# Optimization experiments

Hardware: AMD Instinct MI355X
Metric: run time of the kernel (lower is better)

Reference implementation:

```python
import jax, jax.numpy as jnp
import numpy as np

N = 50000      # num nodes
E = 800000     # num edges (avg degree 16)
D = 128        # feature dim
HOP = 2        # number of propagation hops
FILL = 0.5     # self-loop fill value (A_hat = A + fill*I)


def setup_inputs() -> dict:
    key = jax.random.key(0)
    k1, k2, k3, k4, k5 = jax.random.split(key, 5)
    x_s = jax.random.normal(k1, (N, D), dtype=jnp.float32)
    x_t = jax.random.normal(k2, (N, D), dtype=jnp.float32)
    src = jax.random.randint(k3, (E,), 0, N)
    # guarantee no pre-existing self-loops so that appending all self-loops
    # exactly matches add_remaining_self_loops
    dst = (src + jax.random.randint(k4, (E,), 1, N)) % N
    edge_index = jnp.stack([src, dst]).astype(jnp.int32)
    edge_weight = jax.random.uniform(k5, (E,), dtype=jnp.float32)
    # DIMPA parameters, initialized to 1.0 per _reset_parameters
    w_s = jnp.ones((HOP + 1, 1), dtype=jnp.float32)
    w_t = jnp.ones((HOP + 1, 1), dtype=jnp.float32)
    return {"x_s": x_s, "x_t": x_t, "edge_index": edge_index,
            "edge_weight": edge_weight, "w_s": w_s, "w_t": w_t}


def _conv(x, row, col, w, n, fill):
    # Conv_Base: add self loops with weight `fill`, row-normalize by weighted
    # out-degree of `row`, scatter-add messages w_norm * x[row] onto `col`.
    loop = jnp.arange(n, dtype=row.dtype)
    row_a = jnp.concatenate([row, loop])
    col_a = jnp.concatenate([col, loop])
    w_a = jnp.concatenate([w, jnp.full((n,), fill, dtype=w.dtype)])
    deg = jax.ops.segment_sum(w_a, row_a, num_segments=n)
    deg_inv = jnp.where(deg == 0, jnp.zeros_like(deg), 1.0 / deg)  # inf -> 0
    w_norm = deg_inv[row_a] * w_a                                   # [E+n]
    return jax.ops.segment_sum(w_norm[:, None] * x[row_a], col_a, num_segments=n)


def reference(x_s, x_t, edge_index, edge_weight, w_s, w_t):
    n = x_s.shape[0]
    row, col = edge_index[0], edge_index[1]
    feat_s = w_s[0] * x_s
    feat_t = w_t[0] * x_t
    curr_s, curr_t = x_s, x_t
    for h in range(1, HOP + 1):
        curr_s = _conv(curr_s, row, col, edge_weight, n, FILL)
        # edge_index_t = edge_index[[1, 0]] -> swap row/col
        curr_t = _conv(curr_t, col, row, edge_weight, n, FILL)
        feat_s = feat_s + w_s[h] * curr_s
        feat_t = feat_t + w_t[h] * curr_t
    return jnp.concatenate([feat_s, feat_t], axis=1)  # [N, 2D]
```

## Files before the change

kernel.cpp:

```cpp
#include <hip/hip_runtime.h>

#define D 128
#define FILLV 0.5f
#define NXCD 8
#define EPT 8

#define CNT_SHIFT 22
#define DEG_MASK  0x3FFFFFu

typedef unsigned short u16;
typedef unsigned long long u64;
typedef unsigned uv4 __attribute__((ext_vector_type(4)));

__device__ __forceinline__ u16 f2bf(float f) {
    unsigned u = __float_as_uint(f);
    u += 0x7FFF + ((u >> 16) & 1);
    return (u16)(u >> 16);
}
__device__ __forceinline__ float bf2f(u16 h) {
    return __uint_as_float(((unsigned)h) << 16);
}

__global__ void cnt_tobf_kernel(const int* __restrict__ row, const int* __restrict__ col,
                                const float* __restrict__ w,
                                unsigned* __restrict__ cnt32, unsigned* __restrict__ ranks,
                                const float* __restrict__ x_s, const float* __restrict__ x_t,
                                u16* __restrict__ xb_s, u16* __restrict__ xb_t,
                                int E, int N, int nEB, long long nd) {
    if ((int)blockIdx.x < nEB) {
        long long g  = (long long)blockIdx.x * 256 + threadIdx.x;
        long long e0 = g * EPT;
        if (e0 >= E) return;
        if (e0 + EPT <= E && (E & 3) == 0) {
            int rr[EPT]; int cc[EPT]; unsigned fx[EPT];
            #pragma unroll
            for (int h = 0; h < EPT / 4; ++h) {
                int q = (int)(e0 >> 2) + h;
                int4   r4 = *(const int4*)(row + 4 * (size_t)q);
                int4   c4 = *(const int4*)(col + 4 * (size_t)q);
                float4 w4 = *(const float4*)(w + 4 * (size_t)q);
                rr[4*h] = r4.x; rr[4*h+1] = r4.y; rr[4*h+2] = r4.z; rr[4*h+3] = r4.w;
                cc[4*h] = c4.x; cc[4*h+1] = c4.y; cc[4*h+2] = c4.z; cc[4*h+3] = c4.w;
                fx[4*h]   = (unsigned)(w4.x * 65536.0f);
                fx[4*h+1] = (unsigned)(w4.y * 65536.0f);
                fx[4*h+2] = (unsigned)(w4.z * 65536.0f);
                fx[4*h+3] = (unsigned)(w4.w * 65536.0f);
            }
            unsigned oc[EPT], orr[EPT];
            #pragma unroll
            for (int k = 0; k < EPT; ++k) {
                unsigned add = (1u << CNT_SHIFT) | fx[k];
                oc[k]  = atomicAdd(&cnt32[(size_t)cc[k]], add);
                orr[k] = atomicAdd(&cnt32[(size_t)N + rr[k]], add);
            }
            unsigned pk[EPT];
            #pragma unroll
            for (int k = 0; k < EPT; ++k)
                pk[k] = ((orr[k] >> CNT_SHIFT) << 16) | (oc[k] >> CNT_SHIFT);
            uv4 pa = {pk[0], pk[1], pk[2], pk[3]};
            uv4 pb = {pk[4], pk[5], pk[6], pk[7]};
            __builtin_nontemporal_store(pa, (uv4*)(ranks + e0));
            __builtin_nontemporal_store(pb, (uv4*)(ranks + e0 + 4));
        } else {
            for (long long e = e0; e < E && e < e0 + EPT; ++e) {
                int r = row[e], c = col[e];
                unsigned add = (1u << CNT_SHIFT) | (unsigned)(w[e] * 65536.0f);
                unsigned oc  = atomicAdd(&cnt32[(size_t)c], add);
                unsigned orr = atomicAdd(&cnt32[(size_t)N + r], add);
                ranks[e] = ((orr >> CNT_SHIFT) << 16) | (oc >> CNT_SHIFT);
            }
        }
    } else {
        long long t = (long long)(blockIdx.x - nEB) * 256 + threadIdx.x;
        long long q = nd / 4;
        const float* x; u16* xb; long long i;
        if (t < q) { x = x_s; xb = xb_s; i = t * 4; }
        else if (t < 2 * q) { x = x_t; xb = xb_t; i = (t - q) * 4; }
        else return;
        float4 v = *(const float4*)(x + i);
        ushort4 o;
        o.x = f2bf(v.x); o.y = f2bf(v.y); o.z = f2bf(v.z); o.w = f2bf(v.w);
        *(ushort4*)(xb + i) = o;
    }
}

__global__ void scanAI_kernel(unsigned* __restrict__ cnt32, float* __restrict__ dinv,
                              int* __restrict__ tsum, int total) {
    __shared__ int sh[256];
    int gid = blockIdx.x * 256 + threadIdx.x;
    int cnt = 0;
    if (gid < total) {
        unsigned v = cnt32[gid];
        float deg = (float)(v & DEG_MASK) * (1.0f / 65536.0f);
        dinv[gid] = 1.0f / (deg + FILLV);
        cnt = (int)(v >> CNT_SHIFT);
        cnt32[gid] = (unsigned)cnt;
    }
    sh[threadIdx.x] = cnt;
    __syncthreads();
    for (int off = 128; off > 0; off >>= 1) {
        if (threadIdx.x < off) sh[threadIdx.x] += sh[threadIdx.x + off];
        __syncthreads();
    }
    if (threadIdx.x == 0) tsum[blockIdx.x] = sh[0];
}

__global__ void scanC_kernel(const unsigned* __restrict__ cnt32, const int* __restrict__ tsum,
                             int* __restrict__ start, int total, int grand_total) {
    __shared__ int sh[256];
    int acc = 0;
    for (int j = threadIdx.x; j < (int)blockIdx.x; j += 256) acc += tsum[j];
    sh[threadIdx.x] = acc;
    __syncthreads();
    for (int off = 128; off > 0; off >>= 1) {
        if (threadIdx.x < off) sh[threadIdx.x] += sh[threadIdx.x + off];
        __syncthreads();
    }
    int bpref = sh[0];
    __syncthreads();
    int gid = blockIdx.x * 256 + threadIdx.x;
    int v = (gid < total) ? (int)cnt32[gid] : 0;
    sh[threadIdx.x] = v;
    __syncthreads();
    for (int off = 1; off < 256; off <<= 1) {
        int u = 0;
        if (threadIdx.x >= off) u = sh[threadIdx.x - off];
        __syncthreads();
        sh[threadIdx.x] += u;
        __syncthreads();
    }
    int run = bpref + sh[threadIdx.x] - v;
    if (gid < total) start[gid] = run;
    if (gid == 0) start[total] = grand_total;
}

__global__ void slot_kernel(const int* __restrict__ start,
                            const int* __restrict__ row, const int* __restrict__ col,
                            const float* __restrict__ w, const unsigned* __restrict__ ranks,
                            const float* __restrict__ dinv,
                            u64* __restrict__ ssst, u64* __restrict__ es, u64* __restrict__ et,
                            int E, int N) {
    long long g  = (long long)blockIdx.x * blockDim.x + threadIdx.x;
    long long e0 = g * 4;
    if (e0 >= E) return;
    if (e0 + 4 <= E && (E & 3) == 0) {
        int q = (int)(e0 >> 2);
        int4   r4 = *(const int4*)(row + 4 * (size_t)q);
        int4   c4 = *(const int4*)(col + 4 * (size_t)q);
        float4 w4 = *(const float4*)(w + 4 * (size_t)q);
        uv4    p4 = __builtin_nontemporal_load((const uv4*)(ranks + e0));
        int rr[4] = {r4.x, r4.y, r4.z, r4.w};
        int cc[4] = {c4.x, c4.y, c4.z, c4.w};
        float ww[4] = {w4.x, w4.y, w4.z, w4.w};
        unsigned pk[4] = {p4.x, p4.y, p4.z, p4.w};
        #pragma unroll
        for (int k = 0; k < 4; ++k) {
            int ss = start[cc[k]] + (int)(pk[k] & 0xffffu);
            int st = start[N + rr[k]] + (int)(pk[k] >> 16);
            float wns = ww[k] * dinv[N + rr[k]];
            float wnt = ww[k] * dinv[cc[k]];
            u64 sv = ((u64)(unsigned)st << 32) | (unsigned)ss;
            u64 ev = ((u64)__float_as_uint(wns) << 32) | (unsigned)rr[k];
            u64 tv = ((u64)__float_as_uint(wnt) << 32) | (unsigned)cc[k];
            __builtin_nontemporal_store(sv, ssst + e0 + k);
            __builtin_nontemporal_store(ev, es + e0 + k);
            __builtin_nontemporal_store(tv, et + e0 + k);
        }
    } else {
        for (long long e = e0; e < E && e < e0 + 4; ++e) {
            int r = row[e], c = col[e];
            float we = w[e];
            unsigned pk = ranks[e];
            int ss = start[c] + (int)(pk & 0xffffu);
            int st = start[N + r] + (int)(pk >> 16);
            float wns = we * dinv[N + r];
            float wnt = we * dinv[c];
            __builtin_nontemporal_store(((u64)(unsigned)st << 32) | (unsigned)ss, ssst + e);
            __builtin_nontemporal_store(((u64)__float_as_uint(wns) << 32) | (unsigned)r, es + e);
            __builtin_nontemporal_store(((u64)__float_as_uint(wnt) << 32) | (unsigned)c, et + e);
        }
    }
}

__global__ void fillX_kernel(const u64* __restrict__ ssst,
                             const u64* __restrict__ es, const u64* __restrict__ et,
                             u64* __restrict__ edges, int E, int SL) {
    int e = (int)(blockIdx.x >> 3) * blockDim.x + threadIdx.x;
    int rid = blockIdx.x & 7;
    if (e >= E) return;
    int lo = rid * SL, hi = lo + SL;
    u64 sv = __builtin_nontemporal_load(ssst + e);
    int ss = (int)(unsigned)(sv & 0xffffffffu);
    int st = (int)(unsigned)(sv >> 32);
    bool ds = (ss >= lo) & (ss < hi);
    bool dt = (st >= lo) & (st < hi);
    if (ds) {
        u64 ev = __builtin_nontemporal_load(es + e);
        edges[ss] = ev;
    }
    if (dt) {
        u64 tv = __builtin_nontemporal_load(et + e);
        edges[st] = tv;
    }
}

__global__ void pull1_kernel(const int* __restrict__ start, const int2* __restrict__ edges,
                             const float* __restrict__ dinv,
                             const u16* __restrict__ xb_s, const u16* __restrict__ xb_t,
                             const float* __restrict__ x_s, const float* __restrict__ x_t,
                             u16* __restrict__ ab_s, u16* __restrict__ ab_t, int N) {
    int wid0 = (int)(((long long)blockIdx.x * blockDim.x + threadIdx.x) >> 6);
    int wid = __builtin_amdgcn_readfirstlane(wid0);
    int lane = threadIdx.x & 63;
    int half = lane >> 5, hl = lane & 31;
    if (wid >= 2 * N) return;
    const u16* xb; const float* x; u16* ab; int i, o;
    if (wid < N) { i = wid;     o = N; xb = xb_s; x = x_s; ab = ab_s; }
    else         { i = wid - N; o = 0; xb = xb_t; x = x_t; ab = ab_t; }
    int s0 = start[wid], s1 = start[wid + 1];
    float a0 = 0.f, a1 = 0.f, a2 = 0.f, a3 = 0.f;
    int k = s0;
    for (; k + 8 <= s1; k += 8) {
        int b = k + 4 * half;
        int2 p0 = edges[b], p1 = edges[b + 1], p2 = edges[b + 2], p3 = edges[b + 3];
        ushort4 v0 = *(const ushort4*)(xb + (size_t)p0.x * D + hl * 4);
        ushort4 v1 = *(const ushort4*)(xb + (size_t)p1.x * D + hl * 4);
        ushort4 v2 = *(const ushort4*)(xb + (size_t)p2.x * D + hl * 4);
        ushort4 v3 = *(const ushort4*)(xb + (size_t)p3.x * D + hl * 4);
        float w0v = __int_as_float(p0.y), w1v = __int_as_float(p1.y);
        float w2v = __int_as_float(p2.y), w3v = __int_as_float(p3.y);
        a0 += w0v * bf2f(v0.x) + w1v * bf2f(v1.x) + w2v * bf2f(v2.x) + w3v * bf2f(v3.x);
        a1 += w0v * bf2f(v0.y) + w1v * bf2f(v1.y) + w2v * bf2f(v2.y) + w3v * bf2f(v3.y);
        a2 += w0v * bf2f(v0.z) + w1v * bf2f(v1.z) + w2v * bf2f(v2.z) + w3v * bf2f(v3.z);
        a3 += w0v * bf2f(v0.w) + w1v * bf2f(v1.w) + w2v * bf2f(v2.w) + w3v * bf2f(v3.w);
    }
    if (k + 4 <= s1) {
        int b = k + 2 * half;
        int2 p0 = edges[b], p1 = edges[b + 1];
        ushort4 v0 = *(const ushort4*)(xb + (size_t)p0.x * D + hl * 4);
        ushort4 v1 = *(const ushort4*)(xb + (size_t)p1.x * D + hl * 4);
        float w0v = __int_as_float(p0.y), w1v = __int_as_float(p1.y);
        a0 += w0v * bf2f(v0.x) + w1v * bf2f(v1.x);
        a1 += w0v * bf2f(v0.y) + w1v * bf2f(v1.y);
        a2 += w0v * bf2f(v0.z) + w1v * bf2f(v1.z);
        a3 += w0v * bf2f(v0.w) + w1v * bf2f(v1.w);
        k += 4;
    }
    for (; k < s1; ++k) {
        if (half == 0) {
            int2 p = edges[k];
            ushort4 v = *(const ushort4*)(xb + (size_t)p.x * D + hl * 4);
            float wv = __int_as_float(p.y);
            a0 += wv * bf2f(v.x); a1 += wv * bf2f(v.y);
            a2 += wv * bf2f(v.z); a3 += wv * bf2f(v.w);
        }
    }
    a0 += __shfl_xor(a0, 32); a1 += __shfl_xor(a1, 32);
    a2 += __shfl_xor(a2, 32); a3 += __shfl_xor(a3, 32);
    if (half == 0) {
        float sw = FILLV * dinv[o + i];
        float4 xv = *(const float4*)(x + (size_t)i * D + hl * 4);
        a0 += sw * xv.x; a1 += sw * xv.y; a2 += sw * xv.z; a3 += sw * xv.w;
        ushort4 ov;
        ov.x = f2bf(a0); ov.y = f2bf(a1); ov.z = f2bf(a2); ov.w = f2bf(a3);
        *(ushort4*)(ab + (size_t)i * D + hl * 4) = ov;
    }
}

__global__ void pull2_kernel(const int* __restrict__ start, const int2* __restrict__ edges,
                             const float* __restrict__ dinv,
                             const u16* __restrict__ ab_s, const u16* __restrict__ ab_t,
                             const float* __restrict__ x_s, const float* __restrict__ x_t,
                             float* __restrict__ out,
                             const float* __restrict__ w_s, const float* __restrict__ w_t, int N) {
    int wid0 = (int)(((long long)blockIdx.x * blockDim.x + threadIdx.x) >> 6);
    int wid = __builtin_amdgcn_readfirstlane(wid0);
    int lane = threadIdx.x & 63;
    int half = lane >> 5, hl = lane & 31;
    if (wid >= 2 * N) return;
    const u16* ab; const float* x; const float* wv3; int i, o, hoff;
    if (wid < N) { i = wid;     o = N; ab = ab_s; x = x_s; wv3 = w_s; hoff = 0; }
    else         { i = wid - N; o = 0; ab = ab_t; x = x_t; wv3 = w_t; hoff = D; }
    int s0 = start[wid], s1 = start[wid + 1];
    float a0 = 0.f, a1 = 0.f, a2 = 0.f, a3 = 0.f;
    int k = s0;
    for (; k + 8 <= s1; k += 8) {
        int b = k + 4 * half;
        int2 p0 = edges[b], p1 = edges[b + 1], p2 = edges[b + 2], p3 = edges[b + 3];
        ushort4 v0 = *(const ushort4*)(ab + (size_t)p0.x * D + hl * 4);
        ushort4 v1 = *(const ushort4*)(ab + (size_t)p1.x * D + hl * 4);
        ushort4 v2 = *(const ushort4*)(ab + (size_t)p2.x * D + hl * 4);
        ushort4 v3 = *(const ushort4*)(ab + (size_t)p3.x * D + hl * 4);
        float w0v = __int_as_float(p0.y), w1v = __int_as_float(p1.y);
        float w2v = __int_as_float(p2.y), w3v = __int_as_float(p3.y);
        a0 += w0v * bf2f(v0.x) + w1v * bf2f(v1.x) + w2v * bf2f(v2.x) + w3v * bf2f(v3.x);
        a1 += w0v * bf2f(v0.y) + w1v * bf2f(v1.y) + w2v * bf2f(v2.y) + w3v * bf2f(v3.y);
        a2 += w0v * bf2f(v0.z) + w1v * bf2f(v1.z) + w2v * bf2f(v2.z) + w3v * bf2f(v3.z);
        a3 += w0v * bf2f(v0.w) + w1v * bf2f(v1.w) + w2v * bf2f(v2.w) + w3v * bf2f(v3.w);
    }
    if (k + 4 <= s1) {
        int b = k + 2 * half;
        int2 p0 = edges[b], p1 = edges[b + 1];
        ushort4 v0 = *(const ushort4*)(ab + (size_t)p0.x * D + hl * 4);
        ushort4 v1 = *(const ushort4*)(ab + (size_t)p1.x * D + hl * 4);
        float w0v = __int_as_float(p0.y), w1v = __int_as_float(p1.y);
        a0 += w0v * bf2f(v0.x) + w1v * bf2f(v1.x);
        a1 += w0v * bf2f(v0.y) + w1v * bf2f(v1.y);
        a2 += w0v * bf2f(v0.z) + w1v * bf2f(v1.z);
        a3 += w0v * bf2f(v0.w) + w1v * bf2f(v1.w);
        k += 4;
    }
    for (; k < s1; ++k) {
        if (half == 0) {
            int2 p = edges[k];
            ushort4 v = *(const ushort4*)(ab + (size_t)p.x * D + hl * 4);
            float wv = __int_as_float(p.y);
            a0 += wv * bf2f(v.x); a1 += wv * bf2f(v.y);
            a2 += wv * bf2f(v.z); a3 += wv * bf2f(v.w);
        }
    }
    a0 += __shfl_xor(a0, 32); a1 += __shfl_xor(a1, 32);
    a2 += __shfl_xor(a2, 32); a3 += __shfl_xor(a3, 32);
    if (half == 0) {
        float sw = FILLV * dinv[o + i];
        ushort4 av = *(const ushort4*)(ab + (size_t)i * D + hl * 4);
        float b0 = bf2f(av.x), b1 = bf2f(av.y), b2 = bf2f(av.z), b3 = bf2f(av.w);
        a0 += sw * b0; a1 += sw * b1; a2 += sw * b2; a3 += sw * b3;
        float w0 = wv3[0], w1 = wv3[1], w2 = wv3[2];
        float4 xv = *(const float4*)(x + (size_t)i * D + hl * 4);
        float4 ov;
        ov.x = w0 * xv.x + w1 * b0 + w2 * a0;
        ov.y = w0 * xv.y + w1 * b1 + w2 * a1;
        ov.z = w0 * xv.z + w1 * b2 + w2 * a2;
        ov.w = w0 * xv.w + w1 * b3 + w2 * a3;
        *(float4*)(out + (size_t)i * 2 * D + hoff + hl * 4) = ov;
    }
}

extern "C" void kernel_launch(void* const* d_in, const int* in_sizes, int n_in,
                              void* d_out, int out_size, void* d_ws, size_t ws_size,
                              hipStream_t stream) {
    const float* x_s = (const float*)d_in[0];
    const float* x_t = (const float*)d_in[1];
    const int*   ei  = (const int*)d_in[2];
    const float* ew  = (const float*)d_in[3];
    const float* w_s = (const float*)d_in[4];
    const float* w_t = (const float*)d_in[5];
    const int N = in_sizes[0] / D;
    const int E = in_sizes[3];
    const int* row = ei;
    const int* col = ei + E;

    const int total = 2 * N;
    const int nTiles = (total + 255) / 256;

    float* f      = (float*)d_ws;
    float* dinv   = f;
    int*   start  = (int*)(f + (size_t)total);
    int*   tsum   = start + (total + 2);
    char*  pc     = (char*)(tsum + 512);
    pc = (char*)(((size_t)pc + 255) & ~(size_t)255);
    u64*   edges  = (u64*)pc;
    u16*   xb_s   = (u16*)(edges + 2 * (size_t)E);
    u16*   xb_t   = xb_s + (size_t)N * D;
    u16*   ab_s   = xb_t + (size_t)N * D;
    u16*   ab_t   = ab_s + (size_t)N * D;
    unsigned* cnt32 = (unsigned*)ab_s;

    unsigned* ranks = (unsigned*)d_out;
    char* po = (char*)d_out + (((size_t)E * 4 + 15) & ~(size_t)15);
    u64* ssst = (u64*)po;
    u64* es   = ssst + (size_t)E;
    u64* et   = es + (size_t)E;
    float* out = (float*)d_out;

    hipMemsetAsync(cnt32, 0, (size_t)total * sizeof(unsigned), stream);

    long long nd = (long long)N * D;
    int blkC = (int)((nd / 2 + 255) / 256);
    int blkE = (E + 255) / 256;
    int nEB  = (E + EPT * 256 - 1) / (EPT * 256);
    cnt_tobf_kernel<<<nEB + blkC, 256, 0, stream>>>(row, col, ew, cnt32, ranks,
                                                    x_s, x_t, xb_s, xb_t,
                                                    E, N, nEB, nd);
    scanAI_kernel<<<nTiles, 256, 0, stream>>>(cnt32, dinv, tsum, total);
    scanC_kernel<<<nTiles, 256, 0, stream>>>(cnt32, tsum, start, total, 2 * E);

    int blkS = (E / 4 + 256) / 256 + 1;
    slot_kernel<<<blkS, 256, 0, stream>>>(start, row, col, ew, ranks, dinv,
                                          ssst, es, et, E, N);

    int SL = ((2 * E + NXCD - 1) / NXCD + 7) & ~7;
    fillX_kernel<<<NXCD * blkE, 256, 0, stream>>>(ssst, es, et, edges, E, SL);

    long long pull_threads = (long long)total * 64;
    int blkP = (int)((pull_threads + 255) / 256);
    pull1_kernel<<<blkP, 256, 0, stream>>>(start, (const int2*)edges, dinv, xb_s, xb_t,
                                           x_s, x_t, ab_s, ab_t, N);
    pull2_kernel<<<blkP, 256, 0, stream>>>(start, (const int2*)edges, dinv, ab_s, ab_t,
                                           x_s, x_t, out, w_s, w_t, N);
}
```

Measured before the change: 351.8 us.

## Bucket edge records by destination XCD slice before scatter fill

The slot kernel now bins each edge record by which destination range (one per XCD) its CSR slot falls in, using a shared-memory histogram and global atomic cursors, and writes compact per-bin slot and payload arrays. The fill kernel then reads only its own bin instead of having all 8 range-filtered passes re-scan every edge. This removes the 8x redundant reads of the staging arrays but adds atomics and a non-deterministic write order within bins, and it needs extra cursor memset space.

```diff
diff --git a/kernel.cpp b/kernel.cpp
--- a/kernel.cpp
+++ b/kernel.cpp
@@ -11,6 +11,7 @@
 typedef unsigned short u16;
 typedef unsigned long long u64;
 typedef unsigned uv4 __attribute__((ext_vector_type(4)));
+typedef u64 u64v2 __attribute__((ext_vector_type(2)));
 
 __device__ __forceinline__ u16 f2bf(float f) {
     unsigned u = __float_as_uint(f);
@@ -134,73 +135,95 @@
     if (gid == 0) start[total] = grand_total;
 }
 
-__global__ void slot_kernel(const int* __restrict__ start,
-                            const int* __restrict__ row, const int* __restrict__ col,
-                            const float* __restrict__ w, const unsigned* __restrict__ ranks,
-                            const float* __restrict__ dinv,
-                            u64* __restrict__ ssst, u64* __restrict__ es, u64* __restrict__ et,
-                            int E, int N) {
-    long long g  = (long long)blockIdx.x * blockDim.x + threadIdx.x;
+__global__ void slot2_kernel(const int* __restrict__ start,
+                             const int* __restrict__ row, const int* __restrict__ col,
+                             const float* __restrict__ w, const unsigned* __restrict__ ranks,
+                             const float* __restrict__ dinv,
+                             unsigned* __restrict__ cursor,
+                             unsigned* __restrict__ bslot, u64* __restrict__ bpay,
+                             int E, int N, int SL) {
+    __shared__ unsigned hist[NXCD];
+    __shared__ unsigned wbase[NXCD];
+    if (threadIdx.x < NXCD) hist[threadIdx.x] = 0;
+    __syncthreads();
+    long long g  = (long long)blockIdx.x * 256 + threadIdx.x;
     long long e0 = g * 4;
-    if (e0 >= E) return;
-    if (e0 + 4 <= E && (E & 3) == 0) {
-        int q = (int)(e0 >> 2);
-        int4   r4 = *(const int4*)(row + 4 * (size_t)q);
-        int4   c4 = *(const int4*)(col + 4 * (size_t)q);
-        float4 w4 = *(const float4*)(w + 4 * (size_t)q);
-        uv4    p4 = __builtin_nontemporal_load((const uv4*)(ranks + e0));
-        int rr[4] = {r4.x, r4.y, r4.z, r4.w};
-        int cc[4] = {c4.x, c4.y, c4.z, c4.w};
-        float ww[4] = {w4.x, w4.y, w4.z, w4.w};
-        unsigned pk[4] = {p4.x, p4.y, p4.z, p4.w};
-        #pragma unroll
-        for (int k = 0; k < 4; ++k) {
-            int ss = start[cc[k]] + (int)(pk[k] & 0xffffu);
-            int st = start[N + rr[k]] + (int)(pk[k] >> 16);
-            float wns = ww[k] * dinv[N + rr[k]];
-            float wnt = ww[k] * dinv[cc[k]];
-            u64 sv = ((u64)(unsigned)st << 32) | (unsigned)ss;
-            u64 ev = ((u64)__float_as_uint(wns) << 32) | (unsigned)rr[k];
-            u64 tv = ((u64)__float_as_uint(wnt) << 32) | (unsigned)cc[k];
-            __builtin_nontemporal_store(sv, ssst + e0 + k);
-            __builtin_nontemporal_store(ev, es + e0 + k);
-            __builtin_nontemporal_store(tv, et + e0 + k);
+    unsigned rslot[8]; u64 rpay[8]; unsigned rbin[8], rrank[8];
+    int nrec = 0;
+    if (e0 < E) {
+        if (e0 + 4 <= E && (E & 3) == 0) {
+            int q = (int)(e0 >> 2);
+            int4   r4 = *(const int4*)(row + 4 * (size_t)q);
+            int4   c4 = *(const int4*)(col + 4 * (size_t)q);
+            float4 w4 = *(const float4*)(w + 4 * (size_t)q);
+            uv4    p4 = __builtin_nontemporal_load((const uv4*)(ranks + e0));
+            int rr[4] = {r4.x, r4.y, r4.z, r4.w};
+            int cc[4] = {c4.x, c4.y, c4.z, c4.w};
+            float ww[4] = {w4.x, w4.y, w4.z, w4.w};
+            unsigned pk[4] = {p4.x, p4.y, p4.z, p4.w};
+            #pragma unroll
+            for (int k = 0; k < 4; ++k) {
+                int ss = start[cc[k]] + (int)(pk[k] & 0xffffu);
+                int st = start[N + rr[k]] + (int)(pk[k] >> 16);
+                float wns = ww[k] * dinv[N + rr[k]];
+                float wnt = ww[k] * dinv[cc[k]];
+                rslot[nrec] = (unsigned)ss;
+                rpay[nrec]  = ((u64)__float_as_uint(wns) << 32) | (unsigned)rr[k];
+                ++nrec;
+                rslot[nrec] = (unsigned)st;
+                rpay[nrec]  = ((u64)__float_as_uint(wnt) << 32) | (unsigned)cc[k];
+                ++nrec;
+            }
+        } else {
+            for (long long e = e0; e < E && e < e0 + 4; ++e) {
+                int r = row[e], c = col[e];
+                float we = w[e];
+                unsigned pk = ranks[e];
+                int ss = start[c] + (int)(pk & 0xffffu);
+                int st = start[N + r] + (int)(pk >> 16);
+                float wns = we * dinv[N + r];
+                float wnt = we * dinv[c];
+                rslot[nrec] = (unsigned)ss;
+                rpay[nrec]  = ((u64)__float_as_uint(wns) << 32) | (unsigned)r;
+                ++nrec;
+                rslot[nrec] = (unsigned)st;
+                rpay[nrec]  = ((u64)__float_as_uint(wnt) << 32) | (unsigned)c;
+                ++nrec;
+            }
         }
+        for (int j = 0; j < nrec; ++j) {
+            rbin[j]  = rslot[j] / (unsigned)SL;
+            rrank[j] = atomicAdd(&hist[rbin[j]], 1u);
+        }
+    }
+    __syncthreads();
+    if (threadIdx.x < NXCD)
+        wbase[threadIdx.x] = atomicAdd(&cursor[threadIdx.x], hist[threadIdx.x]);
+    __syncthreads();
+    for (int j = 0; j < nrec; ++j) {
+        unsigned pos = rbin[j] * (unsigned)SL + wbase[rbin[j]] + rrank[j];
+        bslot[pos] = rslot[j];
+        bpay[pos]  = rpay[j];
+    }
+}
+
+__global__ void fill2_kernel(const unsigned* __restrict__ bslot, const u64* __restrict__ bpay,
+                             u64* __restrict__ edges, int E2, int SL) {
+    int rid = blockIdx.x & 7;
+    long long idx = ((long long)(blockIdx.x >> 3) * 256 + threadIdx.x) * 2;
+    long long lo  = (long long)rid * SL;
+    long long rem = (long long)E2 - lo;
+    int cntb = rem < 0 ? 0 : (rem > SL ? SL : (int)rem);
+    if (idx >= cntb) return;
+    long long p = lo + idx;
+    if (idx + 2 <= cntb) {
+        u64   s2 = __builtin_nontemporal_load((const u64*)(bslot + p));
+        u64v2 y2 = __builtin_nontemporal_load((const u64v2*)(bpay + p));
+        unsigned s0 = (unsigned)(s2 & 0xffffffffu), s1 = (unsigned)(s2 >> 32);
+        edges[s0] = y2[0];
+        edges[s1] = y2[1];
     } else {
-        for (long long e = e0; e < E && e < e0 + 4; ++e) {
-            int r = row[e], c = col[e];
-            float we = w[e];
-            unsigned pk = ranks[e];
-            int ss = start[c] + (int)(pk & 0xffffu);
-            int st = start[N + r] + (int)(pk >> 16);
-            float wns = we * dinv[N + r];
-            float wnt = we * dinv[c];
-            __builtin_nontemporal_store(((u64)(unsigned)st << 32) | (unsigned)ss, ssst + e);
-            __builtin_nontemporal_store(((u64)__float_as_uint(wns) << 32) | (unsigned)r, es + e);
-            __builtin_nontemporal_store(((u64)__float_as_uint(wnt) << 32) | (unsigned)c, et + e);
-        }
-    }
-}
-
-__global__ void fillX_kernel(const u64* __restrict__ ssst,
-                             const u64* __restrict__ es, const u64* __restrict__ et,
-                             u64* __restrict__ edges, int E, int SL) {
-    int e = (int)(blockIdx.x >> 3) * blockDim.x + threadIdx.x;
-    int rid = blockIdx.x & 7;
-    if (e >= E) return;
-    int lo = rid * SL, hi = lo + SL;
-    u64 sv = __builtin_nontemporal_load(ssst + e);
-    int ss = (int)(unsigned)(sv & 0xffffffffu);
-    int st = (int)(unsigned)(sv >> 32);
-    bool ds = (ss >= lo) & (ss < hi);
-    bool dt = (st >= lo) & (st < hi);
-    if (ds) {
-        u64 ev = __builtin_nontemporal_load(es + e);
-        edges[ss] = ev;
-    }
-    if (dt) {
-        u64 tv = __builtin_nontemporal_load(et + e);
-        edges[st] = tv;
+        edges[bslot[p]] = __builtin_nontemporal_load(bpay + p);
     }
 }
 
@@ -353,6 +376,7 @@
 
     const int total = 2 * N;
     const int nTiles = (total + 255) / 256;
+    const int SL = ((2 * E + NXCD - 1) / NXCD + 7) & ~7;
 
     float* f      = (float*)d_ws;
     float* dinv   = f;
@@ -365,20 +389,19 @@
     u16*   xb_t   = xb_s + (size_t)N * D;
     u16*   ab_s   = xb_t + (size_t)N * D;
     u16*   ab_t   = ab_s + (size_t)N * D;
-    unsigned* cnt32 = (unsigned*)ab_s;
+    unsigned* cnt32  = (unsigned*)ab_s;
+    unsigned* cursor = cnt32 + (size_t)total;
 
     unsigned* ranks = (unsigned*)d_out;
     char* po = (char*)d_out + (((size_t)E * 4 + 15) & ~(size_t)15);
-    u64* ssst = (u64*)po;
-    u64* es   = ssst + (size_t)E;
-    u64* et   = es + (size_t)E;
+    unsigned* bslot = (unsigned*)po;
+    u64*      bpay  = (u64*)(bslot + (size_t)NXCD * SL);
     float* out = (float*)d_out;
 
-    hipMemsetAsync(cnt32, 0, (size_t)total * sizeof(unsigned), stream);
+    hipMemsetAsync(cnt32, 0, ((size_t)total + NXCD) * sizeof(unsigned), stream);
 
     long long nd = (long long)N * D;
     int blkC = (int)((nd / 2 + 255) / 256);
-    int blkE = (E + 255) / 256;
     int nEB  = (E + EPT * 256 - 1) / (EPT * 256);
     cnt_tobf_kernel<<<nEB + blkC, 256, 0, stream>>>(row, col, ew, cnt32, ranks,
                                                     x_s, x_t, xb_s, xb_t,
@@ -386,12 +409,12 @@
     scanAI_kernel<<<nTiles, 256, 0, stream>>>(cnt32, dinv, tsum, total);
     scanC_kernel<<<nTiles, 256, 0, stream>>>(cnt32, tsum, start, total, 2 * E);
 
-    int blkS = (E / 4 + 256) / 256 + 1;
-    slot_kernel<<<blkS, 256, 0, stream>>>(start, row, col, ew, ranks, dinv,
-                                          ssst, es, et, E, N);
-
-    int SL = ((2 * E + NXCD - 1) / NXCD + 7) & ~7;
-    fillX_kernel<<<NXCD * blkE, 256, 0, stream>>>(ssst, es, et, edges, E, SL);
+    int blkS = (E + 1023) / 1024;
+    slot2_kernel<<<blkS, 256, 0, stream>>>(start, row, col, ew, ranks, dinv,
+                                           cursor, bslot, bpay, E, N, SL);
+
+    int blkF = 8 * ((SL + 511) / 512);
+    fill2_kernel<<<blkF, 256, 0, stream>>>(bslot, bpay, edges, 2 * E, SL);
 
     long long pull_threads = (long long)total * 64;
     int blkP = (int)((pull_threads + 255) / 256);
```

Measured after the change: 337.4 us. 4.1% less time.
